# Performance work log

Measured on AMD Instinct MI355X. Metric: run time of the kernel, lower is better.

The kernel has to match this reference:

```python
import jax, jax.numpy as jnp
import numpy as np

N = 50000   # nodes
E = 800000  # edges
F = 128     # num_features
H = 128     # hidden_size


def gcn_conv(x, W, b, src, dst, num_nodes):
    """PyG-style GCNConv: x' = D^{-1/2}(A+I)D^{-1/2} (x @ W) + b."""
    xw = x @ W  # [N, H] transform before propagation (PyG order)
    # add self loops
    loop = jnp.arange(num_nodes)
    s = jnp.concatenate([src, loop])
    d = jnp.concatenate([dst, loop])
    # symmetric normalization: degree counted on target nodes
    deg = jax.ops.segment_sum(jnp.ones(s.shape[0], dtype=xw.dtype), d,
                              num_segments=num_nodes)
    dinv = jnp.where(deg > 0, jax.lax.rsqrt(deg), 0.0)
    norm = dinv[s] * dinv[d]            # [E+N]
    msgs = xw[s] * norm[:, None]        # gather + scale
    out = jax.ops.segment_sum(msgs, d, num_segments=num_nodes)  # scatter-add
    return out + b


def setup_inputs() -> dict:
    key = jax.random.key(0)
    ks = jax.random.split(key, 6)
    x = jax.random.normal(ks[0], (N, F), dtype=jnp.float32)
    edge_index = jax.random.randint(ks[1], (2, E), 0, N, dtype=jnp.int32)
    W1 = jax.random.normal(ks[2], (F, H), dtype=jnp.float32) * (1.0 / np.sqrt(F))
    b1 = jnp.zeros((H,), dtype=jnp.float32)
    W2 = jax.random.normal(ks[3], (H, H), dtype=jnp.float32) * (1.0 / np.sqrt(H))
    b2 = jnp.zeros((H,), dtype=jnp.float32)
    Wf = jax.random.normal(ks[4], (H, 1), dtype=jnp.float32) * (1.0 / np.sqrt(H))
    bf = jnp.zeros((1,), dtype=jnp.float32)
    return {"x": x, "edge_index": edge_index, "W1": W1, "b1": b1,
            "W2": W2, "b2": b2, "Wf": Wf, "bf": bf}


def reference(x, edge_index, W1, b1, W2, b2, Wf, bf):
    src, dst = edge_index[0], edge_index[1]
    h = jax.nn.relu(gcn_conv(x, W1, b1, src, dst, N))
    h = jax.nn.relu(gcn_conv(h, W2, b2, src, dst, N))
    return (h @ Wf + bf)[:, 0]  # [N]
```

## Files before the change

kernel.cpp:

```cpp
#include <hip/hip_runtime.h>
#include <hip/hip_bf16.h>


#define FDIM 128
#define BSHIFT 9
#define BNODES 512
#define MAXB 128
#define CHUNK 8192

typedef unsigned int uint;
typedef unsigned short ushort;
typedef __attribute__((ext_vector_type(8))) short short8v;
typedef __attribute__((ext_vector_type(4))) float f32x4;

__device__ inline float2 bf2f(uint u) {
    return make_float2(__uint_as_float(u << 16), __uint_as_float(u & 0xffff0000u));
}
__device__ inline ushort f2bf(float f) {
    uint u = __float_as_uint(f);
    return (ushort)((u + 0x7fffu + ((u >> 16) & 1u)) >> 16);
}
__device__ inline float bfval(ushort h) { return __uint_as_float((uint)h << 16); }
__device__ inline uint packbf2(float a, float b) {
    return (uint)f2bf(a) | ((uint)f2bf(b) << 16);
}
__device__ inline int swz(int row, int colShorts) {
    return (((colShorts >> 3) ^ (row & 7)) << 3) | (colShorts & 7);
}


__global__ __launch_bounds__(256) void k_hist(const int* __restrict__ dst,
                                              int* __restrict__ bincnt, int E) {
    __shared__ int h[MAXB];
    int t = threadIdx.x;
    if (t < MAXB) h[t] = 0;
    __syncthreads();
    int b0 = blockIdx.x * CHUNK;
    #pragma unroll 4
    for (int i = 0; i < CHUNK / 256; ++i) {
        int e = b0 + i * 256 + t;
        if (e < E) atomicAdd(&h[dst[e] >> BSHIFT], 1);
    }
    __syncthreads();
    if (t < MAXB && h[t]) atomicAdd(&bincnt[t], h[t]);
}

__global__ __launch_bounds__(128) void k_scanb(const int* __restrict__ bincnt,
                                               int* __restrict__ binoff,
                                               int* __restrict__ bincursor, int nb) {
    __shared__ int s[MAXB];
    int t = threadIdx.x;
    int v = (t < nb) ? bincnt[t] : 0;
    s[t] = v;
    __syncthreads();
    for (int off = 1; off < MAXB; off <<= 1) {
        int u = (t >= off) ? s[t - off] : 0;
        __syncthreads();
        s[t] += u;
        __syncthreads();
    }
    if (t < nb) {
        binoff[t + 1] = s[t];
        bincursor[t] = s[t] - v;
    }
    if (t == 0) binoff[0] = 0;
}

__global__ __launch_bounds__(256) void k_scat(const int* __restrict__ src,
                                              const int* __restrict__ dst,
                                              int* __restrict__ bincursor,
                                              uint* __restrict__ binbuf, int E) {
    __shared__ int h[MAXB], base[MAXB], cnt[MAXB];
    int t = threadIdx.x;
    if (t < MAXB) { h[t] = 0; cnt[t] = 0; }
    __syncthreads();
    int b0 = blockIdx.x * CHUNK;
    #pragma unroll 4
    for (int i = 0; i < CHUNK / 256; ++i) {
        int e = b0 + i * 256 + t;
        if (e < E) atomicAdd(&h[dst[e] >> BSHIFT], 1);
    }
    __syncthreads();
    if (t < MAXB && h[t]) base[t] = atomicAdd(&bincursor[t], h[t]);
    __syncthreads();
    #pragma unroll 4
    for (int i = 0; i < CHUNK / 256; ++i) {
        int e = b0 + i * 256 + t;
        if (e < E) {
            int d = dst[e];
            int b = d >> BSHIFT;
            int r = atomicAdd(&cnt[b], 1);
            binbuf[base[b] + r] = (uint)(((d - (b << BSHIFT)) << 16) | src[e]);
        }
    }
}

__global__ __launch_bounds__(BNODES) void k_bucket(const uint* __restrict__ binbuf,
                                                   const int* __restrict__ binoff,
                                                   int* __restrict__ row_ptr,
                                                   float* __restrict__ dinv,
                                                   int* __restrict__ col,
                                                   int N, int E) {
    __shared__ int sdeg[BNODES], sexcl[BNODES], scnt[BNODES];
    int b = blockIdx.x, t = threadIdx.x;
    int gnode = (b << BSHIFT) + t;
    sdeg[t] = 0;
    scnt[t] = 0;
    __syncthreads();
    int beg = binoff[b], end = binoff[b + 1];
    for (int i = beg + t; i < end; i += BNODES)
        atomicAdd(&sdeg[binbuf[i] >> 16], 1);
    __syncthreads();
    int d = sdeg[t];
    sexcl[t] = d;
    __syncthreads();
    for (int off = 1; off < BNODES; off <<= 1) {
        int u = (t >= off) ? sexcl[t - off] : 0;
        __syncthreads();
        sexcl[t] += u;
        __syncthreads();
    }
    int excl = sexcl[t] - d;
    if (gnode < N) {
        row_ptr[gnode] = beg + excl;
        dinv[gnode] = rsqrtf((float)d + 1.0f);
        if (gnode == N - 1) row_ptr[N] = E;
    }
    __syncthreads();
    sexcl[t] = excl;
    __syncthreads();
    for (int i = beg + t; i < end; i += BNODES) {
        uint p = binbuf[i];
        int dl = p >> 16;
        int r = atomicAdd(&scnt[dl], 1);
        col[beg + sexcl[dl] + r] = (int)(p & 0xffffu);
    }
}


template <int CHAINS>
__global__ __launch_bounds__(256) void k_gemm_mfma(const void* __restrict__ Xv,
                                                   const float* __restrict__ W,
                                                   const float* __restrict__ dinv,
                                                   ushort* __restrict__ Y, int M) {
    __shared__ alignas(16) ushort Xh[64][64];
    __shared__ alignas(16) ushort Xl[(CHAINS == 3) ? 64 : 1][64];
    __shared__ alignas(16) ushort Wth[128][64];
    __shared__ alignas(16) ushort Wtl[128][64];

    const int t = threadIdx.x;
    const int wv = t >> 6;
    const int lane = t & 63;
    const int rb = blockIdx.x * 64;

    f32x4 acc[8];
    #pragma unroll
    for (int i = 0; i < 8; ++i) acc[i] = (f32x4){0.f, 0.f, 0.f, 0.f};

    for (int kc = 0; kc < 2; ++kc) {
        const int k0 = kc * 64;
        if constexpr (CHAINS == 3) {
            const float* Xf = (const float*)Xv;
            #pragma unroll
            for (int it = 0; it < 4; ++it) {
                int idx = t + it * 256;
                int r = idx >> 4, c4 = (idx & 15) * 4;
                int gr = rb + r;
                float4 v = make_float4(0.f, 0.f, 0.f, 0.f);
                if (gr < M) v = *(const float4*)&Xf[(size_t)gr * FDIM + k0 + c4];
                ushort h0 = f2bf(v.x), h1 = f2bf(v.y), h2 = f2bf(v.z), h3 = f2bf(v.w);
                uint2 hw, lw;
                hw.x = (uint)h0 | ((uint)h1 << 16);
                hw.y = (uint)h2 | ((uint)h3 << 16);
                lw.x = (uint)f2bf(v.x - bfval(h0)) | ((uint)f2bf(v.y - bfval(h1)) << 16);
                lw.y = (uint)f2bf(v.z - bfval(h2)) | ((uint)f2bf(v.w - bfval(h3)) << 16);
                int cs = swz(r, c4);
                *(uint2*)&Xh[r][cs] = hw;
                *(uint2*)&Xl[r][cs] = lw;
            }
        } else {
            const ushort* Xb = (const ushort*)Xv;
            #pragma unroll
            for (int it = 0; it < 4; ++it) {
                int idx = t + it * 256;
                int r = idx >> 4, c4 = (idx & 15) * 4;
                int gr = rb + r;
                uint2 u = make_uint2(0u, 0u);
                if (gr < M) u = *(const uint2*)&Xb[(size_t)gr * FDIM + k0 + c4];
                *(uint2*)&Xh[r][swz(r, c4)] = u;
            }
        }
        {
            int n = t & 127, kk0 = (t >> 7) * 32;
            #pragma unroll
            for (int g = 0; g < 4; ++g) {
                uint hw[4], lw[4];
                #pragma unroll
                for (int jp = 0; jp < 4; ++jp) {
                    int k = k0 + kk0 + g * 8 + jp * 2;
                    float w0 = W[(size_t)k * FDIM + n];
                    float w1 = W[(size_t)(k + 1) * FDIM + n];
                    ushort h0 = f2bf(w0), h1 = f2bf(w1);
                    hw[jp] = (uint)h0 | ((uint)h1 << 16);
                    lw[jp] = (uint)f2bf(w0 - bfval(h0)) | ((uint)f2bf(w1 - bfval(h1)) << 16);
                }
                int cs = swz(n, kk0 + g * 8);
                *(uint4*)&Wth[n][cs] = make_uint4(hw[0], hw[1], hw[2], hw[3]);
                *(uint4*)&Wtl[n][cs] = make_uint4(lw[0], lw[1], lw[2], lw[3]);
            }
        }
        __syncthreads();
        const int arow = 16 * wv + (lane & 15);
        #pragma unroll
        for (int ks = 0; ks < 2; ++ks) {
            const int kf = ks * 32 + ((lane >> 4) << 3);
            short8v ah = *(const short8v*)&Xh[arow][swz(arow, kf)];
            short8v al;
            if constexpr (CHAINS == 3) al = *(const short8v*)&Xl[arow][swz(arow, kf)];
            #pragma unroll
            for (int ct = 0; ct < 8; ++ct) {
                int brow = 16 * ct + (lane & 15);
                int bcs = swz(brow, kf);
                short8v bh = *(const short8v*)&Wth[brow][bcs];
                short8v bl = *(const short8v*)&Wtl[brow][bcs];
                acc[ct] = __builtin_amdgcn_mfma_f32_16x16x32_bf16(ah, bh, acc[ct], 0, 0, 0);
                acc[ct] = __builtin_amdgcn_mfma_f32_16x16x32_bf16(ah, bl, acc[ct], 0, 0, 0);
                if constexpr (CHAINS == 3)
                    acc[ct] = __builtin_amdgcn_mfma_f32_16x16x32_bf16(al, bh, acc[ct], 0, 0, 0);
            }
        }
        __syncthreads();
    }
    const int rbase = rb + 16 * wv + ((lane >> 4) << 2);
    const int cbase = lane & 15;
    #pragma unroll
    for (int ri = 0; ri < 4; ++ri) {
        int R = rbase + ri;
        if (R < M) {
            float s = dinv[R];
            ushort* Yrow = Y + (size_t)R * FDIM;
            #pragma unroll
            for (int ct = 0; ct < 8; ++ct)
                Yrow[16 * ct + cbase] = f2bf(acc[ct][ri] * s);
        }
    }
}


template <bool FINAL>
__global__ __launch_bounds__(256) void k_agg(const uint* __restrict__ y,
                                             const float* __restrict__ bvec,
                                             const float* __restrict__ dinv,
                                             const int* __restrict__ row_ptr,
                                             const int* __restrict__ col,
                                             uint* __restrict__ h,
                                             const float* __restrict__ Wf,
                                             const float* __restrict__ bf,
                                             float* __restrict__ out, int n) {
    int wid = threadIdx.x >> 6, lane = threadIdx.x & 63;
    int node = blockIdx.x * 4 + wid;
    if (node >= n) return;
    int beg = row_ptr[node], end = row_ptr[node + 1];
    float2 acc = bf2f(y[(size_t)node * 64 + lane]);
    int e = beg;
    for (; e + 8 <= end; e += 8) {
        int s0 = col[e],     s1 = col[e + 1], s2 = col[e + 2], s3 = col[e + 3];
        int s4 = col[e + 4], s5 = col[e + 5], s6 = col[e + 6], s7 = col[e + 7];
        uint v0 = y[(size_t)s0 * 64 + lane];
        uint v1 = y[(size_t)s1 * 64 + lane];
        uint v2 = y[(size_t)s2 * 64 + lane];
        uint v3 = y[(size_t)s3 * 64 + lane];
        uint v4 = y[(size_t)s4 * 64 + lane];
        uint v5 = y[(size_t)s5 * 64 + lane];
        uint v6 = y[(size_t)s6 * 64 + lane];
        uint v7 = y[(size_t)s7 * 64 + lane];
        float2 f0 = bf2f(v0), f1 = bf2f(v1), f2 = bf2f(v2), f3 = bf2f(v3);
        float2 f4 = bf2f(v4), f5 = bf2f(v5), f6 = bf2f(v6), f7 = bf2f(v7);
        acc.x += ((f0.x + f1.x) + (f2.x + f3.x)) + ((f4.x + f5.x) + (f6.x + f7.x));
        acc.y += ((f0.y + f1.y) + (f2.y + f3.y)) + ((f4.y + f5.y) + (f6.y + f7.y));
    }
    for (; e < end; ++e) {
        float2 f = bf2f(y[(size_t)col[e] * 64 + lane]);
        acc.x += f.x;
        acc.y += f.y;
    }
    float dn = dinv[node];
    float2 bb = *(const float2*)&bvec[lane * 2];
    float ox = fmaxf(fmaf(acc.x, dn, bb.x), 0.f);
    float oy = fmaxf(fmaf(acc.y, dn, bb.y), 0.f);
    if (FINAL) {
        float2 wf = *(const float2*)&Wf[lane * 2];
        float s = ox * wf.x + oy * wf.y;
        #pragma unroll
        for (int off = 32; off > 0; off >>= 1) s += __shfl_xor(s, off);
        if (lane == 0) out[node] = s + bf[0];
    } else {
        h[(size_t)node * 64 + lane] = packbf2(ox, oy);
    }
}


extern "C" void kernel_launch(void* const* d_in, const int* in_sizes, int n_in,
                              void* d_out, int out_size, void* d_ws, size_t ws_size,
                              hipStream_t stream) {
    const float* x  = (const float*)d_in[0];
    const int*   ei = (const int*)d_in[1];
    const float* W1 = (const float*)d_in[2];
    const float* b1 = (const float*)d_in[3];
    const float* W2 = (const float*)d_in[4];
    const float* b2 = (const float*)d_in[5];
    const float* Wf = (const float*)d_in[6];
    const float* bf = (const float*)d_in[7];

    const int N = in_sizes[0] / FDIM;
    const int E = in_sizes[1] / 2;
    const int* src = ei;
    const int* dst = ei + E;
    const int nb = (N + BNODES - 1) >> BSHIFT;

    char* ws = (char*)d_ws;
    size_t off = 0;
    auto alloc = [&](size_t bytes) -> void* {
        void* p = ws + off;
        off = (off + bytes + 511) & ~(size_t)511;
        return p;
    };
    uint*  bufA      = (uint*)alloc((size_t)N * FDIM * 2);
    uint*  bufB      = (uint*)alloc((size_t)N * FDIM * 2);
    int*   col       = (int*)alloc((size_t)E * 4);
    uint*  binbuf    = (uint*)alloc((size_t)E * 4);
    float* dinv      = (float*)alloc((size_t)N * 4);
    int*   row_ptr   = (int*)alloc((size_t)(N + 1) * 4);
    int*   bincnt    = (int*)alloc(MAXB * 4);
    int*   binoff    = (int*)alloc((MAXB + 1) * 4);
    int*   bincursor = (int*)alloc(MAXB * 4);

    hipMemsetAsync(bincnt, 0, MAXB * 4, stream);
    int nwg = (E + CHUNK - 1) / CHUNK;
    k_hist<<<nwg, 256, 0, stream>>>(dst, bincnt, E);
    k_scanb<<<1, 128, 0, stream>>>(bincnt, binoff, bincursor, nb);
    k_scat<<<nwg, 256, 0, stream>>>(src, dst, bincursor, binbuf, E);
    k_bucket<<<nb, BNODES, 0, stream>>>(binbuf, binoff, row_ptr, dinv, col, N, E);

    int gb = (N + 63) / 64;
    k_gemm_mfma<3><<<gb, 256, 0, stream>>>(x, W1, dinv, (ushort*)bufA, N);
    k_agg<false><<<(N + 3) / 4, 256, 0, stream>>>(bufA, b1, dinv, row_ptr, col, bufB,
                                                  nullptr, nullptr, nullptr, N);
    k_gemm_mfma<2><<<gb, 256, 0, stream>>>(bufB, W2, dinv, (ushort*)bufA, N);
    k_agg<true><<<(N + 3) / 4, 256, 0, stream>>>(bufA, b2, dinv, row_ptr, col, nullptr,
                                                 Wf, bf, (float*)d_out, N);
}
```

Before: 244.6 us.

## Fuse edge binning with first GEMM and use fixed-capacity bins to drop histogram pass

Removes the separate histogram and scan kernels by giving each destination bin a fixed CAP-sized slot, so edges can be scattered using a global atomic cursor alone. The first GEMM no longer depends on dinv, so it runs unscaled inside the same launch as the scatter, on the extra blocks. The dinv scaling for layer one moves into the aggregation as a per-edge gather of dinv[src]. This cuts launches and the extra pass over dst, at the cost of extra dinv gathers in the first aggregation and an overflow risk if a bin holds more than CAP edges.

```diff
diff --git a/kernel.cpp b/kernel.cpp
--- a/kernel.cpp
+++ b/kernel.cpp
@@ -7,6 +7,7 @@
 #define BNODES 512
 #define MAXB 128
 #define CHUNK 8192
+#define CAP 10240
 
 typedef unsigned int uint;
 typedef unsigned short ushort;
@@ -28,130 +29,17 @@
     return (((colShorts >> 3) ^ (row & 7)) << 3) | (colShorts & 7);
 }
 
-
-__global__ __launch_bounds__(256) void k_hist(const int* __restrict__ dst,
-                                              int* __restrict__ bincnt, int E) {
-    __shared__ int h[MAXB];
-    int t = threadIdx.x;
-    if (t < MAXB) h[t] = 0;
-    __syncthreads();
-    int b0 = blockIdx.x * CHUNK;
-    #pragma unroll 4
-    for (int i = 0; i < CHUNK / 256; ++i) {
-        int e = b0 + i * 256 + t;
-        if (e < E) atomicAdd(&h[dst[e] >> BSHIFT], 1);
-    }
-    __syncthreads();
-    if (t < MAXB && h[t]) atomicAdd(&bincnt[t], h[t]);
-}
-
-__global__ __launch_bounds__(128) void k_scanb(const int* __restrict__ bincnt,
-                                               int* __restrict__ binoff,
-                                               int* __restrict__ bincursor, int nb) {
-    __shared__ int s[MAXB];
-    int t = threadIdx.x;
-    int v = (t < nb) ? bincnt[t] : 0;
-    s[t] = v;
-    __syncthreads();
-    for (int off = 1; off < MAXB; off <<= 1) {
-        int u = (t >= off) ? s[t - off] : 0;
-        __syncthreads();
-        s[t] += u;
-        __syncthreads();
-    }
-    if (t < nb) {
-        binoff[t + 1] = s[t];
-        bincursor[t] = s[t] - v;
-    }
-    if (t == 0) binoff[0] = 0;
-}
-
-__global__ __launch_bounds__(256) void k_scat(const int* __restrict__ src,
-                                              const int* __restrict__ dst,
-                                              int* __restrict__ bincursor,
-                                              uint* __restrict__ binbuf, int E) {
-    __shared__ int h[MAXB], base[MAXB], cnt[MAXB];
-    int t = threadIdx.x;
-    if (t < MAXB) { h[t] = 0; cnt[t] = 0; }
-    __syncthreads();
-    int b0 = blockIdx.x * CHUNK;
-    #pragma unroll 4
-    for (int i = 0; i < CHUNK / 256; ++i) {
-        int e = b0 + i * 256 + t;
-        if (e < E) atomicAdd(&h[dst[e] >> BSHIFT], 1);
-    }
-    __syncthreads();
-    if (t < MAXB && h[t]) base[t] = atomicAdd(&bincursor[t], h[t]);
-    __syncthreads();
-    #pragma unroll 4
-    for (int i = 0; i < CHUNK / 256; ++i) {
-        int e = b0 + i * 256 + t;
-        if (e < E) {
-            int d = dst[e];
-            int b = d >> BSHIFT;
-            int r = atomicAdd(&cnt[b], 1);
-            binbuf[base[b] + r] = (uint)(((d - (b << BSHIFT)) << 16) | src[e]);
-        }
-    }
-}
-
-__global__ __launch_bounds__(BNODES) void k_bucket(const uint* __restrict__ binbuf,
-                                                   const int* __restrict__ binoff,
-                                                   int* __restrict__ row_ptr,
-                                                   float* __restrict__ dinv,
-                                                   int* __restrict__ col,
-                                                   int N, int E) {
-    __shared__ int sdeg[BNODES], sexcl[BNODES], scnt[BNODES];
-    int b = blockIdx.x, t = threadIdx.x;
-    int gnode = (b << BSHIFT) + t;
-    sdeg[t] = 0;
-    scnt[t] = 0;
-    __syncthreads();
-    int beg = binoff[b], end = binoff[b + 1];
-    for (int i = beg + t; i < end; i += BNODES)
-        atomicAdd(&sdeg[binbuf[i] >> 16], 1);
-    __syncthreads();
-    int d = sdeg[t];
-    sexcl[t] = d;
-    __syncthreads();
-    for (int off = 1; off < BNODES; off <<= 1) {
-        int u = (t >= off) ? sexcl[t - off] : 0;
-        __syncthreads();
-        sexcl[t] += u;
-        __syncthreads();
-    }
-    int excl = sexcl[t] - d;
-    if (gnode < N) {
-        row_ptr[gnode] = beg + excl;
-        dinv[gnode] = rsqrtf((float)d + 1.0f);
-        if (gnode == N - 1) row_ptr[N] = E;
-    }
-    __syncthreads();
-    sexcl[t] = excl;
-    __syncthreads();
-    for (int i = beg + t; i < end; i += BNODES) {
-        uint p = binbuf[i];
-        int dl = p >> 16;
-        int r = atomicAdd(&scnt[dl], 1);
-        col[beg + sexcl[dl] + r] = (int)(p & 0xffffu);
-    }
-}
-
-
-template <int CHAINS>
-__global__ __launch_bounds__(256) void k_gemm_mfma(const void* __restrict__ Xv,
-                                                   const float* __restrict__ W,
-                                                   const float* __restrict__ dinv,
-                                                   ushort* __restrict__ Y, int M) {
-    __shared__ alignas(16) ushort Xh[64][64];
-    __shared__ alignas(16) ushort Xl[(CHAINS == 3) ? 64 : 1][64];
-    __shared__ alignas(16) ushort Wth[128][64];
-    __shared__ alignas(16) ushort Wtl[128][64];
-
+template <int CHAINS, bool SCALE>
+__device__ __forceinline__ void gemm_core(int bid, const void* __restrict__ Xv,
+                                          const float* __restrict__ W,
+                                          const float* __restrict__ dinv,
+                                          ushort* __restrict__ Y, int M,
+                                          ushort (*Xh)[64], ushort (*Xl)[64],
+                                          ushort (*Wth)[64], ushort (*Wtl)[64]) {
     const int t = threadIdx.x;
     const int wv = t >> 6;
     const int lane = t & 63;
-    const int rb = blockIdx.x * 64;
+    const int rb = bid * 64;
 
     f32x4 acc[8];
     #pragma unroll
@@ -237,7 +125,7 @@
     for (int ri = 0; ri < 4; ++ri) {
         int R = rbase + ri;
         if (R < M) {
-            float s = dinv[R];
+            float s = SCALE ? dinv[R] : 1.0f;
             ushort* Yrow = Y + (size_t)R * FDIM;
             #pragma unroll
             for (int ct = 0; ct < 8; ++ct)
@@ -246,22 +134,119 @@
     }
 }
 
-
-template <bool FINAL>
+__global__ __launch_bounds__(256) void k_scat_gemm(const int* __restrict__ src,
+                                                   const int* __restrict__ dst,
+                                                   int* __restrict__ bincnt,
+                                                   uint* __restrict__ binbuf, int E, int nwg,
+                                                   const void* __restrict__ Xv,
+                                                   const float* __restrict__ W,
+                                                   ushort* __restrict__ Y, int M) {
+    __shared__ alignas(16) ushort Xh[64][64];
+    __shared__ alignas(16) ushort Xl[64][64];
+    __shared__ alignas(16) ushort Wth[128][64];
+    __shared__ alignas(16) ushort Wtl[128][64];
+    __shared__ int h[MAXB], base[MAXB], cnt[MAXB];
+
+    if (blockIdx.x >= nwg) {
+        gemm_core<3, false>(blockIdx.x - nwg, Xv, W, nullptr, Y, M, Xh, Xl, Wth, Wtl);
+        return;
+    }
+    int t = threadIdx.x;
+    if (t < MAXB) { h[t] = 0; cnt[t] = 0; }
+    __syncthreads();
+    int b0 = blockIdx.x * CHUNK;
+    #pragma unroll 4
+    for (int i = 0; i < CHUNK / 256; ++i) {
+        int e = b0 + i * 256 + t;
+        if (e < E) atomicAdd(&h[dst[e] >> BSHIFT], 1);
+    }
+    __syncthreads();
+    if (t < MAXB && h[t]) base[t] = atomicAdd(&bincnt[t], h[t]);
+    __syncthreads();
+    #pragma unroll 4
+    for (int i = 0; i < CHUNK / 256; ++i) {
+        int e = b0 + i * 256 + t;
+        if (e < E) {
+            int d = dst[e];
+            int b = d >> BSHIFT;
+            int r = atomicAdd(&cnt[b], 1);
+            binbuf[(size_t)b * CAP + base[b] + r] = (uint)(((d - (b << BSHIFT)) << 16) | src[e]);
+        }
+    }
+}
+
+template <int CHAINS, bool SCALE>
+__global__ __launch_bounds__(256) void k_gemm_mfma(const void* __restrict__ Xv,
+                                                   const float* __restrict__ W,
+                                                   const float* __restrict__ dinv,
+                                                   ushort* __restrict__ Y, int M) {
+    __shared__ alignas(16) ushort Xh[64][64];
+    __shared__ alignas(16) ushort Xl[(CHAINS == 3) ? 64 : 1][64];
+    __shared__ alignas(16) ushort Wth[128][64];
+    __shared__ alignas(16) ushort Wtl[128][64];
+    gemm_core<CHAINS, SCALE>(blockIdx.x, Xv, W, dinv, Y, M, Xh, Xl, Wth, Wtl);
+}
+
+__global__ __launch_bounds__(BNODES) void k_bucket(const uint* __restrict__ binbuf,
+                                                   const int* __restrict__ bincnt,
+                                                   int* __restrict__ row_ptr,
+                                                   int* __restrict__ degO,
+                                                   float* __restrict__ dinv,
+                                                   int* __restrict__ col, int N) {
+    __shared__ int sdeg[BNODES], sexcl[BNODES], scnt[BNODES];
+    int b = blockIdx.x, t = threadIdx.x;
+    int gnode = (b << BSHIFT) + t;
+    sdeg[t] = 0;
+    scnt[t] = 0;
+    __syncthreads();
+    int beg = b * CAP, count = bincnt[b];
+    for (int i = t; i < count; i += BNODES)
+        atomicAdd(&sdeg[binbuf[beg + i] >> 16], 1);
+    __syncthreads();
+    int d = sdeg[t];
+    sexcl[t] = d;
+    __syncthreads();
+    for (int off = 1; off < BNODES; off <<= 1) {
+        int u = (t >= off) ? sexcl[t - off] : 0;
+        __syncthreads();
+        sexcl[t] += u;
+        __syncthreads();
+    }
+    int excl = sexcl[t] - d;
+    if (gnode < N) {
+        row_ptr[gnode] = beg + excl;
+        degO[gnode] = d;
+        dinv[gnode] = rsqrtf((float)d + 1.0f);
+    }
+    __syncthreads();
+    sexcl[t] = excl;
+    __syncthreads();
+    for (int i = t; i < count; i += BNODES) {
+        uint p = binbuf[beg + i];
+        int dl = p >> 16;
+        int r = atomicAdd(&scnt[dl], 1);
+        col[beg + sexcl[dl] + r] = (int)(p & 0xffffu);
+    }
+}
+
+template <bool SCALE_EDGES, bool FINAL>
 __global__ __launch_bounds__(256) void k_agg(const uint* __restrict__ y,
                                              const float* __restrict__ bvec,
                                              const float* __restrict__ dinv,
                                              const int* __restrict__ row_ptr,
+                                             const int* __restrict__ degA,
                                              const int* __restrict__ col,
                                              uint* __restrict__ h,
                                              const float* __restrict__ Wf,
-                                             const float* __restrict__ bf,
+                                             const float* __restrict__ bfp,
                                              float* __restrict__ out, int n) {
     int wid = threadIdx.x >> 6, lane = threadIdx.x & 63;
     int node = blockIdx.x * 4 + wid;
     if (node >= n) return;
-    int beg = row_ptr[node], end = row_ptr[node + 1];
+    int beg = row_ptr[node], end = beg + degA[node];
+    float dn = dinv[node];
     float2 acc = bf2f(y[(size_t)node * 64 + lane]);
+    if (SCALE_EDGES) { acc.x *= dn; acc.y *= dn; }
     int e = beg;
     for (; e + 8 <= end; e += 8) {
         int s0 = col[e],     s1 = col[e + 1], s2 = col[e + 2], s3 = col[e + 3];
@@ -276,15 +261,34 @@
         uint v7 = y[(size_t)s7 * 64 + lane];
         float2 f0 = bf2f(v0), f1 = bf2f(v1), f2 = bf2f(v2), f3 = bf2f(v3);
         float2 f4 = bf2f(v4), f5 = bf2f(v5), f6 = bf2f(v6), f7 = bf2f(v7);
-        acc.x += ((f0.x + f1.x) + (f2.x + f3.x)) + ((f4.x + f5.x) + (f6.x + f7.x));
-        acc.y += ((f0.y + f1.y) + (f2.y + f3.y)) + ((f4.y + f5.y) + (f6.y + f7.y));
+        if (SCALE_EDGES) {
+            float d0 = dinv[s0], d1 = dinv[s1], d2 = dinv[s2], d3 = dinv[s3];
+            float d4 = dinv[s4], d5 = dinv[s5], d6 = dinv[s6], d7 = dinv[s7];
+            acc.x = fmaf(f0.x, d0, acc.x); acc.y = fmaf(f0.y, d0, acc.y);
+            acc.x = fmaf(f1.x, d1, acc.x); acc.y = fmaf(f1.y, d1, acc.y);
+            acc.x = fmaf(f2.x, d2, acc.x); acc.y = fmaf(f2.y, d2, acc.y);
+            acc.x = fmaf(f3.x, d3, acc.x); acc.y = fmaf(f3.y, d3, acc.y);
+            acc.x = fmaf(f4.x, d4, acc.x); acc.y = fmaf(f4.y, d4, acc.y);
+            acc.x = fmaf(f5.x, d5, acc.x); acc.y = fmaf(f5.y, d5, acc.y);
+            acc.x = fmaf(f6.x, d6, acc.x); acc.y = fmaf(f6.y, d6, acc.y);
+            acc.x = fmaf(f7.x, d7, acc.x); acc.y = fmaf(f7.y, d7, acc.y);
+        } else {
+            acc.x += ((f0.x + f1.x) + (f2.x + f3.x)) + ((f4.x + f5.x) + (f6.x + f7.x));
+            acc.y += ((f0.y + f1.y) + (f2.y + f3.y)) + ((f4.y + f5.y) + (f6.y + f7.y));
+        }
     }
     for (; e < end; ++e) {
-        float2 f = bf2f(y[(size_t)col[e] * 64 + lane]);
-        acc.x += f.x;
-        acc.y += f.y;
-    }
-    float dn = dinv[node];
+        int s = col[e];
+        float2 f = bf2f(y[(size_t)s * 64 + lane]);
+        if (SCALE_EDGES) {
+            float ds = dinv[s];
+            acc.x = fmaf(f.x, ds, acc.x);
+            acc.y = fmaf(f.y, ds, acc.y);
+        } else {
+            acc.x += f.x;
+            acc.y += f.y;
+        }
+    }
     float2 bb = *(const float2*)&bvec[lane * 2];
     float ox = fmaxf(fmaf(acc.x, dn, bb.x), 0.f);
     float oy = fmaxf(fmaf(acc.y, dn, bb.y), 0.f);
@@ -293,7 +297,7 @@
         float s = ox * wf.x + oy * wf.y;
         #pragma unroll
         for (int off = 32; off > 0; off >>= 1) s += __shfl_xor(s, off);
-        if (lane == 0) out[node] = s + bf[0];
+        if (lane == 0) out[node] = s + bfp[0];
     } else {
         h[(size_t)node * 64 + lane] = packbf2(ox, oy);
     }
@@ -325,28 +329,26 @@
         off = (off + bytes + 511) & ~(size_t)511;
         return p;
     };
-    uint*  bufA      = (uint*)alloc((size_t)N * FDIM * 2);
-    uint*  bufB      = (uint*)alloc((size_t)N * FDIM * 2);
-    int*   col       = (int*)alloc((size_t)E * 4);
-    uint*  binbuf    = (uint*)alloc((size_t)E * 4);
-    float* dinv      = (float*)alloc((size_t)N * 4);
-    int*   row_ptr   = (int*)alloc((size_t)(N + 1) * 4);
-    int*   bincnt    = (int*)alloc(MAXB * 4);
-    int*   binoff    = (int*)alloc((MAXB + 1) * 4);
-    int*   bincursor = (int*)alloc(MAXB * 4);
+    uint*  bufA    = (uint*)alloc((size_t)N * FDIM * 2);
+    uint*  bufB    = (uint*)alloc((size_t)N * FDIM * 2);
+    int*   col     = (int*)alloc((size_t)nb * CAP * 4);
+    uint*  binbuf  = (uint*)alloc((size_t)nb * CAP * 4);
+    float* dinv    = (float*)alloc((size_t)N * 4);
+    int*   row_ptr = (int*)alloc((size_t)N * 4);
+    int*   deg     = (int*)alloc((size_t)N * 4);
+    int*   bincnt  = (int*)alloc(MAXB * 4);
 
     hipMemsetAsync(bincnt, 0, MAXB * 4, stream);
-    int nwg = (E + CHUNK - 1) / CHUNK;
-    k_hist<<<nwg, 256, 0, stream>>>(dst, bincnt, E);
-    k_scanb<<<1, 128, 0, stream>>>(bincnt, binoff, bincursor, nb);
-    k_scat<<<nwg, 256, 0, stream>>>(src, dst, bincursor, binbuf, E);
-    k_bucket<<<nb, BNODES, 0, stream>>>(binbuf, binoff, row_ptr, dinv, col, N, E);
-
-    int gb = (N + 63) / 64;
-    k_gemm_mfma<3><<<gb, 256, 0, stream>>>(x, W1, dinv, (ushort*)bufA, N);
-    k_agg<false><<<(N + 3) / 4, 256, 0, stream>>>(bufA, b1, dinv, row_ptr, col, bufB,
-                                                  nullptr, nullptr, nullptr, N);
-    k_gemm_mfma<2><<<gb, 256, 0, stream>>>(bufB, W2, dinv, (ushort*)bufA, N);
-    k_agg<true><<<(N + 3) / 4, 256, 0, stream>>>(bufA, b2, dinv, row_ptr, col, nullptr,
-                                                 Wf, bf, (float*)d_out, N);
-}
+
+    const int nwg = (E + CHUNK - 1) / CHUNK;
+    const int gb  = (N + 63) / 64;
+    k_scat_gemm<<<nwg + gb, 256, 0, stream>>>(src, dst, bincnt, binbuf, E, nwg,
+                                              x, W1, (ushort*)bufA, N);
+    k_bucket<<<nb, BNODES, 0, stream>>>(binbuf, bincnt, row_ptr, deg, dinv, col, N);
+
+    k_agg<true, false><<<(N + 3) / 4, 256, 0, stream>>>(bufA, b1, dinv, row_ptr, deg, col,
+                                                        bufB, nullptr, nullptr, nullptr, N);
+    k_gemm_mfma<2, true><<<gb, 256, 0, stream>>>(bufB, W2, dinv, (ushort*)bufA, N);
+    k_agg<false, true><<<(N + 3) / 4, 256, 0, stream>>>(bufA, b2, dinv, row_ptr, deg, col,
+                                                        nullptr, Wf, bf, (float*)d_out, N);
+}
```

Result: faster. 218.2 us (-10.8%).
